# Performance work log

Hardware: AMD Instinct MI355X
Metric: run time of the kernel (lower is better)

## Reference

```python
import jax, jax.numpy as jnp
import numpy as np

LEAKY_SLOPE = 0.01  # torch nn.LeakyReLU / F.leaky_relu default


def gcn_diffusion(adj, order, feat):
    # A_gcn = adj + I; sym-normalized diffusion D^-1/2 A D^-1/2 applied repeatedly
    B, N, _ = adj.shape
    A = adj + jnp.eye(N, dtype=adj.dtype)
    dinv_sqrt = jnp.sum(A, axis=2) ** -0.5  # [B, N]
    outs = []
    h = feat
    for _ in range(order):
        h = jnp.matmul(A, dinv_sqrt[..., None] * h) * dinv_sqrt[..., None]
        outs.append(h)
    return outs


def scattering_s4(adj, feat):
    # lazy random walk P = 1/2 (I + A D^-1); wavelets Psi_j = P^{2^{j-1}} - P^{2^j}
    dinv = 1.0 / jnp.sum(adj, axis=2)  # [B, N]
    p = feat
    us = []
    for _ in range(8):  # powers P^1 .. P^8
        p = 0.5 * p + 0.5 * jnp.matmul(adj, dinv[..., None] * p)
        us.append(p)
    h1 = feat - us[0]      # I - P
    h2 = us[0] - us[1]     # P - P^2
    h3 = us[1] - us[3]     # P^2 - P^4
    h4 = us[3] - us[7]     # P^4 - P^8
    return h1, h2, h3, h4


def sctconv(X, adj, W1, b1, W2, b2, a, moment):
    leaky = lambda x: jax.nn.leaky_relu(x, LEAKY_SLOPE)
    h = X  # [B, N, F]
    hA, hA2, hA3 = gcn_diffusion(adj, 3, X)
    hA, hA2, hA3 = leaky(hA), leaky(hA2), leaky(hA3)
    s1, s2, s3, s4 = scattering_s4(adj, X)
    mom = jnp.asarray(moment, dtype=X.dtype)
    s1 = jnp.abs(s1) ** mom
    s2 = jnp.abs(s2) ** mom
    s3 = jnp.abs(s3) ** mom
    s4 = jnp.abs(s4) ** mom
    # NOTE: original concatenates only (hA, hA2, s1..s4) -> 6 branches; hA3 is unused.
    h_all = jnp.stack([hA, hA2, s1, s2, s3, s4], axis=1)  # [B, 6, N, F]
    h_b = jnp.broadcast_to(h[:, None], h_all.shape)        # [B, 6, N, F]
    a_input = jnp.concatenate([h_b, h_all], axis=3)        # [B, 6, N, 2F]
    e = jnp.einsum('bknc,c->bkn', jax.nn.relu(a_input), a[:, 0])  # [B, 6, N]
    attention = jax.nn.softmax(e, axis=1)[..., None]       # [B, 6, N, 1]
    h_prime = jnp.mean(attention * h_all, axis=1)          # [B, N, F]
    out = leaky(h_prime @ W1.T + b1)
    out = leaky(out @ W2.T + b2)
    return out


def setup_inputs() -> dict:
    key = jax.random.key(0)
    kx, ka, k1, k2, k3, k4, k5 = jax.random.split(key, 7)
    B, N, F = 8, 4096, 64
    X = jax.random.normal(kx, (B, N, F), dtype=jnp.float32)
    adj = jax.random.uniform(ka, (B, N, N), dtype=jnp.float32)
    s = 1.0 / np.sqrt(F)
    W1 = jax.random.uniform(k1, (F, F), minval=-s, maxval=s, dtype=jnp.float32)
    b1 = jax.random.uniform(k2, (F,), minval=-s, maxval=s, dtype=jnp.float32)
    W2 = jax.random.uniform(k3, (F, F), minval=-s, maxval=s, dtype=jnp.float32)
    b2 = jax.random.uniform(k4, (F,), minval=-s, maxval=s, dtype=jnp.float32)
    a = jax.random.normal(k5, (2 * F, 1), dtype=jnp.float32) * 0.1
    return {"X": X, "adj": adj, "W1": W1, "b1": b1, "W2": W2, "b2": b2, "a": a, "moment": 1}


def reference(X, adj, W1, b1, W2, b2, a, moment):
    return sctconv(X, adj, W1, b1, W2, b2, a, moment)
```

## Files before the change

kernel.cpp:

```cpp
#include <hip/hip_runtime.h>
#include <hip/hip_bf16.h>
#include <cstdio>
#include <cstdint>

#define BB 8
#define NN 4096
#define FF 64

typedef __attribute__((ext_vector_type(8))) short bf16x8;
typedef __attribute__((ext_vector_type(4))) float f32x4;

__device__ __forceinline__ unsigned short f2bf(float f){
  unsigned int u = __float_as_uint(f);
  u += 0x7FFFu + ((u >> 16) & 1u);
  return (unsigned short)(u >> 16);
}

__device__ __forceinline__ float leaky01(float x){ return x > 0.f ? x : 0.01f * x; }

__global__ __launch_bounds__(256) void k_convert(const float* __restrict__ adj,
    unsigned short* __restrict__ At, float* __restrict__ dinv, float* __restrict__ dsq)
{
  const int bid = blockIdx.x;
  const int b = bid & 7, mt = bid >> 3, m0 = mt * 32;
  const int tid = threadIdx.x;
  const int r = tid >> 3, g = tid & 7;
  const float* src = adj + ((size_t)b * NN + m0 + r) * NN + ((g ^ (r & 7)) << 3);
  unsigned short* dst = At + (size_t)bid * 64 * 2048 + (tid << 3);
  float s = 0.f;
  for (int t = 0; t < 64; ++t){
    const float* p = src + t * 64;
    float4 a = *(const float4*)p;
    float4 c = *(const float4*)(p + 4);
    s += ((a.x + a.y) + (a.z + a.w)) + ((c.x + c.y) + (c.z + c.w));
    bf16x8 v;
    v[0] = (short)f2bf(a.x); v[1] = (short)f2bf(a.y); v[2] = (short)f2bf(a.z); v[3] = (short)f2bf(a.w);
    v[4] = (short)f2bf(c.x); v[5] = (short)f2bf(c.y); v[6] = (short)f2bf(c.z); v[7] = (short)f2bf(c.w);
    *(bf16x8*)(dst + (size_t)t * 2048) = v;
  }
  s += __shfl_xor(s, 1); s += __shfl_xor(s, 2); s += __shfl_xor(s, 4);
  if (g == 0){
    dinv[(size_t)b * NN + m0 + r] = 1.0f / s;
    dsq [(size_t)b * NN + m0 + r] = 1.0f / sqrtf(s + 1.0f);
  }
}

__global__ __launch_bounds__(256) void k_prep(const float* __restrict__ X,
    const float* __restrict__ dinv, const float* __restrict__ dsq,
    unsigned short* __restrict__ vt)
{
  const int b = blockIdx.y, n0 = blockIdx.x * 64, tid = threadIdx.x;
  __shared__ unsigned short tg[64][65], ts[64][65];
  #pragma unroll
  for (int i = 0; i < 4; ++i){
    int idx = i * 256 + tid, n = idx >> 4, c4 = (idx & 15) * 4;
    size_t rb = (size_t)b * NN + n0 + n;
    float4 x = *(const float4*)(X + rb * 64 + c4);
    float di = dinv[b * NN + n0 + n], dv = dsq[b * NN + n0 + n];
    tg[c4 + 0][n] = f2bf(dv * x.x); tg[c4 + 1][n] = f2bf(dv * x.y);
    tg[c4 + 2][n] = f2bf(dv * x.z); tg[c4 + 3][n] = f2bf(dv * x.w);
    ts[c4 + 0][n] = f2bf(di * x.x); ts[c4 + 1][n] = f2bf(di * x.y);
    ts[c4 + 2][n] = f2bf(di * x.z); ts[c4 + 3][n] = f2bf(di * x.w);
  }
  __syncthreads();
  #pragma unroll
  for (int i = 0; i < 4; ++i){
    int idx = i * 256 + tid, c = idx >> 4, n4 = (idx & 15) * 4;
    *(ushort4*)(vt + ((size_t)b * 128 + c) * NN + n0 + n4) =
        make_ushort4(tg[c][n4], tg[c][n4 + 1], tg[c][n4 + 2], tg[c][n4 + 3]);
    *(ushort4*)(vt + ((size_t)b * 128 + 64 + c) * NN + n0 + n4) =
        make_ushort4(ts[c][n4], ts[c][n4 + 1], ts[c][n4 + 2], ts[c][n4 + 3]);
  }
}

template<int NC>
__global__ __launch_bounds__(256, 4) void k_gemm_fused(
    const unsigned short* __restrict__ At,
    const unsigned short* __restrict__ vtR, int c0,
    const float* __restrict__ sprev, float* __restrict__ P, float* __restrict__ snap,
    const float* __restrict__ dinv, int writeVtS,
    const float* __restrict__ gprev, float* __restrict__ gout,
    const float* __restrict__ dsq, int writeVtG,
    unsigned short* __restrict__ vtW)
{
  constexpr int NF = NC / 64;
  constexpr int BI = NC / 32;
  __shared__ __align__(16) unsigned short As[2][32 * 64];
  __shared__ __align__(16) unsigned short Bs[2][NC * 64];
  const int bid = blockIdx.x;
  const int b = bid & 7, mt = bid >> 3, m0 = mt * 32;
  const int tid = threadIdx.x;
  const int w = tid >> 6, l = tid & 63;
  const unsigned short* Atile = At + (size_t)bid * 64 * 2048;
  const unsigned short* Bg = vtR + ((size_t)b * 128 + c0) * NN;

  auto stage = [&](int buf, int t){
    {
      const unsigned short* gp = Atile + (size_t)t * 2048 + (tid << 3);
      __builtin_amdgcn_global_load_lds((const __attribute__((address_space(1))) void*)gp,
          (__attribute__((address_space(3))) void*)(&As[buf][tid << 3]), 16, 0, 0);
    }
    #pragma unroll
    for (int i = 0; i < BI; ++i){
      int idx = i * 256 + tid, c = idx >> 3, g = idx & 7;
      const unsigned short* gp = Bg + (size_t)c * NN + t * 64 + ((g ^ (c & 7)) << 3);
      __builtin_amdgcn_global_load_lds((const __attribute__((address_space(1))) void*)gp,
          (__attribute__((address_space(3))) void*)(&Bs[buf][idx << 3]), 16, 0, 0);
    }
  };

  f32x4 acc[2][NF];
  #pragma unroll
  for (int mi = 0; mi < 2; ++mi)
    #pragma unroll
    for (int ni = 0; ni < NF; ++ni)
      #pragma unroll
      for (int j = 0; j < 4; ++j) acc[mi][ni][j] = 0.f;

  stage(0, 0);
  const int r0 = l & 15, hq = l >> 4, sw = r0 & 7;
  constexpr int NT = NN / 64;
  for (int t = 0; t < NT; ++t){
    const int cur = t & 1;
    if (t + 1 < NT){
      stage(cur ^ 1, t + 1);
      if constexpr (NC == 128) asm volatile("s_waitcnt vmcnt(5)" ::: "memory");
      else                     asm volatile("s_waitcnt vmcnt(3)" ::: "memory");
    } else {
      asm volatile("s_waitcnt vmcnt(0)" ::: "memory");
    }
    __builtin_amdgcn_s_barrier();
    asm volatile("" ::: "memory");
    #pragma unroll
    for (int kk = 0; kk < 2; ++kk){
      const int g8 = ((kk * 4 + hq) ^ sw) << 3;
      bf16x8 af[2], bfr[NF];
      #pragma unroll
      for (int mi = 0; mi < 2; ++mi)
        af[mi] = *(const bf16x8*)&As[cur][(mi * 16 + r0) * 64 + g8];
      #pragma unroll
      for (int ni = 0; ni < NF; ++ni)
        bfr[ni] = *(const bf16x8*)&Bs[cur][(w * 16 * NF + ni * 16 + r0) * 64 + g8];
      #pragma unroll
      for (int mi = 0; mi < 2; ++mi)
        #pragma unroll
        for (int ni = 0; ni < NF; ++ni)
          acc[mi][ni] = __builtin_amdgcn_mfma_f32_16x16x32_bf16(af[mi], bfr[ni], acc[mi][ni], 0, 0, 0);
    }
    asm volatile("" ::: "memory");
    __builtin_amdgcn_s_barrier();
    asm volatile("" ::: "memory");
  }

  const bool isScat = (NC == 64) || (w >= 2);
  if (isScat){
    const int wS = (NC == 64) ? w : (w - 2);
    #pragma unroll
    for (int mi = 0; mi < 2; ++mi){
      const int rb = m0 + mi * 16 + hq * 4;
      const size_t rowb = (size_t)b * NN + rb;
      float4 dv4 = *(const float4*)(dinv + (size_t)b * NN + rb);
      #pragma unroll
      for (int ni = 0; ni < NF; ++ni){
        const int cs = wS * 16 * NF + ni * 16 + r0;
        float pn[4];
        #pragma unroll
        for (int j = 0; j < 4; ++j){
          float pv = sprev[(rowb + j) * 64 + cs];
          pn[j] = 0.5f * (pv + acc[mi][ni][j]);
          P[(rowb + j) * 64 + cs] = pn[j];
        }
        if (snap){
          #pragma unroll
          for (int j = 0; j < 4; ++j) snap[(rowb + j) * 64 + cs] = pn[j];
        }
        if (writeVtS){
          ushort4 vv = make_ushort4(f2bf(dv4.x * pn[0]), f2bf(dv4.y * pn[1]),
                                    f2bf(dv4.z * pn[2]), f2bf(dv4.w * pn[3]));
          *(ushort4*)(vtW + ((size_t)b * 128 + 64 + cs) * NN + rb) = vv;
        }
      }
    }
  }
  if constexpr (NC == 128){
    if (!isScat){
      #pragma unroll
      for (int mi = 0; mi < 2; ++mi){
        const int rb = m0 + mi * 16 + hq * 4;
        const size_t rowb = (size_t)b * NN + rb;
        float4 dq4 = *(const float4*)(dsq + (size_t)b * NN + rb);
        #pragma unroll
        for (int ni = 0; ni < NF; ++ni){
          const int cg = w * 16 * NF + ni * 16 + r0;
          float hn[4];
          const float dq[4] = {dq4.x, dq4.y, dq4.z, dq4.w};
          #pragma unroll
          for (int j = 0; j < 4; ++j){
            float hv = gprev[(rowb + j) * 64 + cg];
            hn[j] = (acc[mi][ni][j] + dq[j] * hv) * dq[j];
            gout[(rowb + j) * 64 + cg] = hn[j];
          }
          if (writeVtG){
            ushort4 vv = make_ushort4(f2bf(dq[0] * hn[0]), f2bf(dq[1] * hn[1]),
                                      f2bf(dq[2] * hn[2]), f2bf(dq[3] * hn[3]));
            *(ushort4*)(vtW + ((size_t)b * 128 + cg) * NN + rb) = vv;
          }
        }
      }
    }
  }
}

__global__ __launch_bounds__(256) void k_attn(
    const float* __restrict__ X,  const float* __restrict__ hA, const float* __restrict__ hA2,
    const float* __restrict__ U1, const float* __restrict__ U2, const float* __restrict__ U4,
    const float* __restrict__ U8, const float* __restrict__ W1, const float* __restrict__ b1,
    const float* __restrict__ W2, const float* __restrict__ b2, const float* __restrict__ av,
    const int* __restrict__ momp, float* __restrict__ out)
{
  __shared__ float W1s[64][65], W2s[64][65];
  __shared__ float a1s[64], a2s[64], b1s[64], b2s[64];
  __shared__ float hp[4][64], o1[4][64];
  const int tid = threadIdx.x;
  for (int e = tid; e < 4096; e += 256){
    W1s[e >> 6][e & 63] = W1[e];
    W2s[e >> 6][e & 63] = W2[e];
  }
  if (tid < 64){ a1s[tid] = av[tid]; a2s[tid] = av[64 + tid]; b1s[tid] = b1[tid]; b2s[tid] = b2[tid]; }
  __syncthreads();
  const int w = tid >> 6, l = tid & 63;
  size_t row = (size_t)blockIdx.x * 4 + w;
  size_t off = row * 64 + l;
  float x  = X[off];
  float u1 = U1[off], u2 = U2[off], u4 = U4[off], u8 = U8[off];
  float br[6];
  br[0] = leaky01(hA[off]);
  br[1] = leaky01(hA2[off]);
  float d1 = fabsf(x - u1), d2 = fabsf(u1 - u2), d3 = fabsf(u2 - u4), d4 = fabsf(u4 - u8);
  int mom = *momp;
  if (mom == 1){ br[2] = d1; br[3] = d2; br[4] = d3; br[5] = d4; }
  else {
    float m = (float)mom;
    br[2] = powf(d1, m); br[3] = powf(d2, m); br[4] = powf(d3, m); br[5] = powf(d4, m);
  }
  float v = fmaxf(x, 0.f) * a1s[l];
  for (int o = 32; o; o >>= 1) v += __shfl_xor(v, o);
  float base = v;
  float e[6];
  #pragma unroll
  for (int k = 0; k < 6; ++k){
    float t = fmaxf(br[k], 0.f) * a2s[l];
    for (int o = 32; o; o >>= 1) t += __shfl_xor(t, o);
    e[k] = base + t;
  }
  float mx = e[0];
  #pragma unroll
  for (int k = 1; k < 6; ++k) mx = fmaxf(mx, e[k]);
  float s = 0.f, att[6];
  #pragma unroll
  for (int k = 0; k < 6; ++k){ att[k] = expf(e[k] - mx); s += att[k]; }
  float inv = 1.0f / (6.0f * s);
  float hpv = 0.f;
  #pragma unroll
  for (int k = 0; k < 6; ++k) hpv += att[k] * br[k];
  hpv *= inv;
  hp[w][l] = hpv;
  __syncthreads();
  float acc = b1s[l];
  #pragma unroll 8
  for (int c = 0; c < 64; ++c) acc += hp[w][c] * W1s[l][c];
  o1[w][l] = leaky01(acc);
  __syncthreads();
  float acc2 = b2s[l];
  #pragma unroll 8
  for (int c = 0; c < 64; ++c) acc2 += o1[w][c] * W2s[l][c];
  out[off] = leaky01(acc2);
}

static constexpr size_t OFF_ADJB = 0;
static constexpr size_t OFF_VTA  = OFF_ADJB + (size_t)BB * NN * NN * 2;
static constexpr size_t OFF_VTB  = OFF_VTA  + (size_t)BB * 128 * NN * 2;
static constexpr size_t OFF_HA   = OFF_VTB  + (size_t)BB * 128 * NN * 2;
static constexpr size_t OFF_HA2  = OFF_HA   + (size_t)BB * NN * 64 * 4;
static constexpr size_t OFF_P    = OFF_HA2  + (size_t)BB * NN * 64 * 4;
static constexpr size_t OFF_U1   = OFF_P    + (size_t)BB * NN * 64 * 4;
static constexpr size_t OFF_U2   = OFF_U1   + (size_t)BB * NN * 64 * 4;
static constexpr size_t OFF_U4   = OFF_U2   + (size_t)BB * NN * 64 * 4;
static constexpr size_t OFF_U8   = OFF_U4   + (size_t)BB * NN * 64 * 4;
static constexpr size_t OFF_DINV = OFF_U8   + (size_t)BB * NN * 64 * 4;
static constexpr size_t OFF_DS   = OFF_DINV + (size_t)BB * NN * 4;
static constexpr size_t WS_NEED  = OFF_DS   + (size_t)BB * NN * 4;

extern "C" void kernel_launch(void* const* d_in, const int* in_sizes, int n_in,
                              void* d_out, int out_size, void* d_ws, size_t ws_size,
                              hipStream_t stream)
{
  const float* X   = (const float*)d_in[0];
  const float* adj = (const float*)d_in[1];
  const float* W1  = (const float*)d_in[2];
  const float* b1  = (const float*)d_in[3];
  const float* W2  = (const float*)d_in[4];
  const float* b2  = (const float*)d_in[5];
  const float* av  = (const float*)d_in[6];
  const int*  momp = (const int*)d_in[7];
  float* out = (float*)d_out;

  if (ws_size < WS_NEED){
    fprintf(stderr, "kernel_launch: workspace too small: %zu < %zu\n", ws_size, WS_NEED);
    return;
  }
  char* w = (char*)d_ws;
  unsigned short* At  = (unsigned short*)(w + OFF_ADJB);
  unsigned short* vtA = (unsigned short*)(w + OFF_VTA);
  unsigned short* vtB = (unsigned short*)(w + OFF_VTB);
  float* hA   = (float*)(w + OFF_HA);
  float* hA2  = (float*)(w + OFF_HA2);
  float* P    = (float*)(w + OFF_P);
  float* U1   = (float*)(w + OFF_U1);
  float* U2   = (float*)(w + OFF_U2);
  float* U4   = (float*)(w + OFF_U4);
  float* U8   = (float*)(w + OFF_U8);
  float* dinv = (float*)(w + OFF_DINV);
  float* dsq  = (float*)(w + OFF_DS);

  k_convert<<<1024, 256, 0, stream>>>(adj, At, dinv, dsq);
  dim3 tg64(NN / 64, BB);
  k_prep<<<tg64, 256, 0, stream>>>(X, dinv, dsq, vtA);

  k_gemm_fused<128><<<1024, 256, 0, stream>>>(At, vtA, 0,
      X, P, U1, dinv, 1, X, hA, dsq, 1, vtB);
  k_gemm_fused<128><<<1024, 256, 0, stream>>>(At, vtB, 0,
      P, P, U2, dinv, 1, hA, hA2, dsq, 0, vtA);
  unsigned short* vr = vtA;
  unsigned short* vw = vtB;
  for (int k = 3; k <= 8; ++k){
    float* snap = (k == 4) ? U4 : nullptr;
    float* pdst = (k == 8) ? U8 : P;
    k_gemm_fused<64><<<1024, 256, 0, stream>>>(At, vr, 64,
        P, pdst, snap, dinv, (k < 8) ? 1 : 0, nullptr, nullptr, nullptr, 0, vw);
    unsigned short* t = vr; vr = vw; vw = t;
  }

  k_attn<<<BB * NN / 4, 256, 0, stream>>>(X, hA, hA2, U1, U2, U4, U8,
                                          W1, b1, W2, b2, av, momp, out);
}
```

Measured before the change: 772.9 us.

## Load B operand straight from global into registers, bypassing LDS

The B operand (transposed feature tiles) is no longer staged through shared memory. Each wave loads its own B fragments directly from global memory into registers, double-buffered in pb0/pb1, while A stays in LDS. The loop is manually unrolled by two so each buffer is addressed statically. This removes B LDS traffic and shared-memory footprint, possibly raising occupancy, at the cost of more VGPRs and less coalesced per-lane 16-byte global loads. The vmcnt wait counts were kept although the number of outstanding loads per stage changed, so correctness of the waits is uncertain.

```diff
diff --git a/kernel.cpp b/kernel.cpp
--- a/kernel.cpp
+++ b/kernel.cpp
@@ -84,31 +84,22 @@
     unsigned short* __restrict__ vtW)
 {
   constexpr int NF = NC / 64;
-  constexpr int BI = NC / 32;
   __shared__ __align__(16) unsigned short As[2][32 * 64];
-  __shared__ __align__(16) unsigned short Bs[2][NC * 64];
   const int bid = blockIdx.x;
   const int b = bid & 7, mt = bid >> 3, m0 = mt * 32;
   const int tid = threadIdx.x;
   const int w = tid >> 6, l = tid & 63;
+  const int r0 = l & 15, hq = l >> 4, sw = r0 & 7;
   const unsigned short* Atile = At + (size_t)bid * 64 * 2048;
-  const unsigned short* Bg = vtR + ((size_t)b * 128 + c0) * NN;
-
-  auto stage = [&](int buf, int t){
-    {
-      const unsigned short* gp = Atile + (size_t)t * 2048 + (tid << 3);
-      __builtin_amdgcn_global_load_lds((const __attribute__((address_space(1))) void*)gp,
-          (__attribute__((address_space(3))) void*)(&As[buf][tid << 3]), 16, 0, 0);
-    }
-    #pragma unroll
-    for (int i = 0; i < BI; ++i){
-      int idx = i * 256 + tid, c = idx >> 3, g = idx & 7;
-      const unsigned short* gp = Bg + (size_t)c * NN + t * 64 + ((g ^ (c & 7)) << 3);
-      __builtin_amdgcn_global_load_lds((const __attribute__((address_space(1))) void*)gp,
-          (__attribute__((address_space(3))) void*)(&Bs[buf][idx << 3]), 16, 0, 0);
-    }
+  const unsigned short* Bb = vtR + ((size_t)b * 128 + c0 + w * 16 * NF + r0) * NN + hq * 8;
+
+  auto stageA = [&](int buf, int t){
+    const unsigned short* gp = Atile + (size_t)t * 2048 + (tid << 3);
+    __builtin_amdgcn_global_load_lds((const __attribute__((address_space(1))) void*)gp,
+        (__attribute__((address_space(3))) void*)(&As[buf][tid << 3]), 16, 0, 0);
   };
 
+  bf16x8 pb0[NF][2], pb1[NF][2];
   f32x4 acc[2][NF];
   #pragma unroll
   for (int mi = 0; mi < 2; ++mi)
@@ -117,13 +108,46 @@
       #pragma unroll
       for (int j = 0; j < 4; ++j) acc[mi][ni][j] = 0.f;
 
-  stage(0, 0);
-  const int r0 = l & 15, hq = l >> 4, sw = r0 & 7;
-  constexpr int NT = NN / 64;
-  for (int t = 0; t < NT; ++t){
-    const int cur = t & 1;
-    if (t + 1 < NT){
-      stage(cur ^ 1, t + 1);
+  stageA(0, 0);
+  #pragma unroll
+  for (int ni = 0; ni < NF; ++ni)
+    #pragma unroll
+    for (int kk = 0; kk < 2; ++kk)
+      pb0[ni][kk] = *(const bf16x8*)(Bb + (size_t)ni * 16 * NN + kk * 32);
+
+  #pragma unroll 1
+  for (int t = 0; t < 64; t += 2){
+    stageA(1, t + 1);
+    #pragma unroll
+    for (int ni = 0; ni < NF; ++ni)
+      #pragma unroll
+      for (int kk = 0; kk < 2; ++kk)
+        pb1[ni][kk] = *(const bf16x8*)(Bb + (size_t)ni * 16 * NN + (t + 1) * 64 + kk * 32);
+    if constexpr (NC == 128) asm volatile("s_waitcnt vmcnt(5)" ::: "memory");
+    else                     asm volatile("s_waitcnt vmcnt(3)" ::: "memory");
+    __builtin_amdgcn_s_barrier();
+    asm volatile("" ::: "memory");
+    #pragma unroll
+    for (int kk = 0; kk < 2; ++kk){
+      const int g8 = ((kk * 4 + hq) ^ sw) << 3;
+      bf16x8 af0 = *(const bf16x8*)&As[0][(r0) * 64 + g8];
+      bf16x8 af1 = *(const bf16x8*)&As[0][(16 + r0) * 64 + g8];
+      #pragma unroll
+      for (int ni = 0; ni < NF; ++ni){
+        acc[0][ni] = __builtin_amdgcn_mfma_f32_16x16x32_bf16(af0, pb0[ni][kk], acc[0][ni], 0, 0, 0);
+        acc[1][ni] = __builtin_amdgcn_mfma_f32_16x16x32_bf16(af1, pb0[ni][kk], acc[1][ni], 0, 0, 0);
+      }
+    }
+    asm volatile("" ::: "memory");
+    __builtin_amdgcn_s_barrier();
+    asm volatile("" ::: "memory");
+    if (t + 2 < 64){
+      stageA(0, t + 2);
+      #pragma unroll
+      for (int ni = 0; ni < NF; ++ni)
+        #pragma unroll
+        for (int kk = 0; kk < 2; ++kk)
+          pb0[ni][kk] = *(const bf16x8*)(Bb + (size_t)ni * 16 * NN + (t + 2) * 64 + kk * 32);
       if constexpr (NC == 128) asm volatile("s_waitcnt vmcnt(5)" ::: "memory");
       else                     asm volatile("s_waitcnt vmcnt(3)" ::: "memory");
     } else {
@@ -134,18 +158,13 @@
     #pragma unroll
     for (int kk = 0; kk < 2; ++kk){
       const int g8 = ((kk * 4 + hq) ^ sw) << 3;
-      bf16x8 af[2], bfr[NF];
-      #pragma unroll
-      for (int mi = 0; mi < 2; ++mi)
-        af[mi] = *(const bf16x8*)&As[cur][(mi * 16 + r0) * 64 + g8];
-      #pragma unroll
-      for (int ni = 0; ni < NF; ++ni)
-        bfr[ni] = *(const bf16x8*)&Bs[cur][(w * 16 * NF + ni * 16 + r0) * 64 + g8];
-      #pragma unroll
-      for (int mi = 0; mi < 2; ++mi)
-        #pragma unroll
-        for (int ni = 0; ni < NF; ++ni)
-          acc[mi][ni] = __builtin_amdgcn_mfma_f32_16x16x32_bf16(af[mi], bfr[ni], acc[mi][ni], 0, 0, 0);
+      bf16x8 af0 = *(const bf16x8*)&As[1][(r0) * 64 + g8];
+      bf16x8 af1 = *(const bf16x8*)&As[1][(16 + r0) * 64 + g8];
+      #pragma unroll
+      for (int ni = 0; ni < NF; ++ni){
+        acc[0][ni] = __builtin_amdgcn_mfma_f32_16x16x32_bf16(af0, pb1[ni][kk], acc[0][ni], 0, 0, 0);
+        acc[1][ni] = __builtin_amdgcn_mfma_f32_16x16x32_bf16(af1, pb1[ni][kk], acc[1][ni], 0, 0, 0);
+      }
     }
     asm volatile("" ::: "memory");
     __builtin_amdgcn_s_barrier();
```

After: 975.7 us. 26.2% more time.
